# Kernel tuning notes

Hardware: AMD Instinct MI355X
Metric: run time of the kernel (lower is better)

## Reference

```python
import jax, jax.numpy as jnp
import numpy as np

IOU_THRESHOLD = 0.5
CLASS_CONF_THRESHOLD = 0.01
MAX_OUTPUT = 100  # tf.image.non_max_suppression max_output_size


def _nms_indices(boxes, scores, max_out, iou_thr):
    """Fixed-size greedy NMS: returns (idxs[max_out], valid[max_out])."""
    x1, y1, x2, y2 = boxes[:, 0], boxes[:, 1], boxes[:, 2], boxes[:, 3]
    areas = (x2 - x1) * (y2 - y1)

    def body(sc, _):
        i = jnp.argmax(sc)
        valid = sc[i] > 0.0  # score_threshold = 0.0 in tf call
        xx1 = jnp.maximum(x1[i], x1)
        yy1 = jnp.maximum(y1[i], y1)
        xx2 = jnp.minimum(x2[i], x2)
        yy2 = jnp.minimum(y2[i], y2)
        inter = jnp.maximum(xx2 - xx1, 0.0) * jnp.maximum(yy2 - yy1, 0.0)
        union = areas[i] + areas - inter
        iou = jnp.where(union > 0.0, inter / union, 0.0)
        # suppress overlapping boxes (self included, iou=1) only if pick valid
        sc_new = jnp.where((iou > iou_thr) & valid, -1.0, sc)
        return sc_new, (i, valid)

    _, (idxs, valids) = jax.lax.scan(body, scores, None, length=max_out)
    return idxs, valids


def _decode(x, anchors):
    B, H, W, A, C = x.shape  # B == 1
    gw = jnp.float32(W)
    # grid offsets: (col, row) per cell, matching cell_x / transposed cell_y
    cx = jnp.broadcast_to(jnp.arange(W, dtype=jnp.float32).reshape(1, 1, W, 1, 1), (1, H, W, 1, 1))
    cy = jnp.broadcast_to(jnp.arange(H, dtype=jnp.float32).reshape(1, H, 1, 1, 1), (1, H, W, 1, 1))
    grid = jnp.concatenate([cx, cy], axis=-1)  # (1,H,W,1,2)

    xy = (jax.nn.sigmoid(x[..., 0:2]) + grid) / gw                      # (B,H,W,A,2)
    wh = jnp.exp(x[..., 2:4]) * anchors.reshape(1, 1, 1, A, 2) / gw     # (B,H,W,A,2)
    boxes = jnp.concatenate([xy - wh / 2.0, xy + wh / 2.0], axis=-1)    # (B,H,W,A,4)

    conf = jax.nn.sigmoid(x[..., 4:5])                                  # (B,H,W,A,1)
    cls_prob = jax.nn.softmax(x[..., 5:], axis=-1)                      # (B,H,W,A,C-5)
    class_confidence = conf * cls_prob
    masked = jnp.where(class_confidence > CLASS_CONF_THRESHOLD, class_confidence, 0.0)
    classes = jnp.argmax(masked, axis=-1).astype(jnp.int32)             # (B,H,W,A)
    confm = jnp.max(masked, axis=-1)                                    # (B,H,W,A)

    N = H * W * A
    return boxes.reshape(N, 4), confm.reshape(N), classes.reshape(N)


def reference(x, anchors):
    boxes, scores, classes = _decode(x, anchors)
    idxs, valids = _nms_indices(jax.lax.stop_gradient(boxes),
                                jax.lax.stop_gradient(scores),
                                MAX_OUTPUT, IOU_THRESHOLD)
    sel_conf = jnp.where(valids, scores[idxs], 0.0)
    sel_boxes = jnp.where(valids[:, None], boxes[idxs], 0.0)
    sel_classes = jnp.where(valids, classes[idxs], -1)
    return sel_conf, sel_boxes, sel_classes


def setup_inputs() -> dict:
    key = jax.random.key(0)
    k1, k2 = jax.random.split(key)
    x = jax.random.normal(k1, (1, 256, 256, 5, 85), dtype=jnp.float32)
    # anchor priors in grid units (positive widths/heights)
    anchors = jax.random.uniform(k2, (5, 2), dtype=jnp.float32) * 4.0 + 0.5
    return {"x": x, "anchors": anchors}
```

## Files before the change

kernel.cpp:

```cpp
#include <hip/hip_runtime.h>
#include <hip/hip_bf16.h>

#define NROW 327680
#define NCLS 80
#define K_TARGET 1024u
#define CAP 2048u
#define MAXN 2048
#define MAX_OUT 100
#define NBIN 864
#define BIN0 0x3C23
#define HIST_BLOCKS 80
#define ADJW 32
#define ADJC_ROWS 128

#define WS_SCORES 0
#define WS_PART   1310720
#define WS_CNT    1587200
#define WS_KEYS   1587264
#define WS_SORT   1603648
#define WS_CBOX   1620032
#define WS_ADJ    1652800

typedef float f4v __attribute__((ext_vector_type(4)));
typedef f4v f4u __attribute__((aligned(4)));
typedef unsigned long long ull;

__global__ __launch_bounds__(256, 1) void decode_score(
    const float* __restrict__ x, float* __restrict__ scores) {
  const int r = blockIdx.x * 256 + threadIdx.x;
  const float* rp = x + (size_t)r * 85;

  float conf_l = rp[4];
  float cl[80];
  #pragma unroll
  for (int c = 0; c < 20; ++c) {
    f4v t4 = *(const f4u*)(rp + 5 + 4 * c);
    cl[4*c+0] = t4.x; cl[4*c+1] = t4.y; cl[4*c+2] = t4.z; cl[4*c+3] = t4.w;
  }

  float m = cl[0];
  #pragma unroll
  for (int c = 1; c < NCLS; ++c) { float l = cl[c]; if (l > m) m = l; }
  float s = 0.f;
  #pragma unroll
  for (int c = 0; c < NCLS; ++c) s += expf(cl[c] - m);
  float conf = 1.f / (1.f + expf(-conf_l));
  float best = conf * (1.f / s);
  scores[r] = (best > 0.01f) ? best : 0.f;
}

__global__ __launch_bounds__(1024) void hist_kernel(
    const float* __restrict__ scores, unsigned* __restrict__ part) {
  __shared__ unsigned h[NBIN];
  const int t = threadIdx.x;
  if (t < NBIN) h[t] = 0;
  __syncthreads();

  float4 s4 = ((const float4*)scores)[blockIdx.x * 1024 + t];
  float sv[4] = {s4.x, s4.y, s4.z, s4.w};
  #pragma unroll
  for (int k = 0; k < 4; ++k) {
    float s = sv[k];
    if (s > 0.f) {
      int idx = (int)(__float_as_uint(s) >> 16) - BIN0;
      if (idx > NBIN - 1) idx = NBIN - 1;
      atomicAdd(&h[idx], 1u);
    }
  }
  __syncthreads();
  if (t < NBIN) part[blockIdx.x * NBIN + t] = h[t];
}

__global__ __launch_bounds__(1024) void thresh_kernel(
    const unsigned* __restrict__ part, unsigned* __restrict__ cnt) {
  __shared__ unsigned bufA[1024], bufB[1024];
  const int t = threadIdx.x;

  unsigned colsum = 0;
  if (t < NBIN) {
    unsigned a0 = 0, a1 = 0, a2 = 0, a3 = 0;
    #pragma unroll
    for (int b = 0; b < HIST_BLOCKS; b += 4) {
      a0 += part[(b + 0) * NBIN + t];
      a1 += part[(b + 1) * NBIN + t];
      a2 += part[(b + 2) * NBIN + t];
      a3 += part[(b + 3) * NBIN + t];
    }
    colsum = a0 + a1 + a2 + a3;
  }
  bufA[t] = colsum;
  __syncthreads();

  unsigned* src = bufA; unsigned* dst = bufB;
  for (int d = 1; d < 1024; d <<= 1) {
    unsigned val = src[t] + ((t + d < 1024) ? src[t + d] : 0u);
    dst[t] = val;
    __syncthreads();
    unsigned* tmp = src; src = dst; dst = tmp;
  }
  if (src[t] >= K_TARGET && (t == 1023 || src[t + 1] < K_TARGET)) {
    unsigned T = (unsigned)t;
    if (src[t] > CAP) T += 1;
    cnt[1] = T;
  }
  if (t == 0) {
    if (src[0] < K_TARGET) cnt[1] = 0;
    cnt[0] = 0;
  }
}

__global__ __launch_bounds__(256) void compact_kernel(
    const float* __restrict__ scores, unsigned* __restrict__ cnt,
    ull* __restrict__ keys) {
  __shared__ unsigned blocal, bbase;
  const int t = threadIdx.x;
  if (t == 0) blocal = 0;
  __syncthreads();

  const unsigned T = cnt[1];
  const int gi = blockIdx.x * 256 + t;
  float4 s4 = ((const float4*)scores)[gi];
  float sv[4] = {s4.x, s4.y, s4.z, s4.w};
  ull lk[4]; int nl = 0;
  #pragma unroll
  for (int k = 0; k < 4; ++k) {
    float s = sv[k];
    if (s <= 0.f) continue;
    unsigned bits = __float_as_uint(s);
    int idx = (int)(bits >> 16) - BIN0;
    if (idx > NBIN - 1) idx = NBIN - 1;
    if ((unsigned)idx < T) continue;
    unsigned r = (unsigned)(gi * 4 + k);
    lk[nl++] = ((ull)bits << 32) | (ull)(0xFFFFFFFFu - r);
  }
  unsigned lpos = nl ? atomicAdd(&blocal, (unsigned)nl) : 0u;
  __syncthreads();
  if (t == 0 && blocal) bbase = atomicAdd(&cnt[0], blocal);
  __syncthreads();
  if (nl) {
    unsigned base = bbase + lpos;
    for (int i = 0; i < nl; ++i)
      if (base + i < CAP) keys[base + i] = lk[i];
  }
}

__global__ __launch_bounds__(64) void rank_kernel(
    const float* __restrict__ x, const float* __restrict__ anchors,
    const unsigned* __restrict__ cnt, const ull* __restrict__ keys,
    ull* __restrict__ sorted, float4* __restrict__ cboxg) {
  __shared__ ull lk[MAXN];
  unsigned n = cnt[0]; if (n > CAP) n = CAP;
  const int t = threadIdx.x;
  for (unsigned i = t; i < n; i += 64) lk[i] = keys[i];
  __syncthreads();

  const unsigned i = blockIdx.x * 64 + t;
  if (i >= n) return;
  const ull ki = lk[i];
  unsigned rank = 0;
  #pragma unroll 4
  for (unsigned j = 0; j < n; ++j) rank += (lk[j] > ki) ? 1u : 0u;

  sorted[rank] = ki;

  unsigned r = 0xFFFFFFFFu - (unsigned)(ki & 0xFFFFFFFFull);
  const float* rp = x + (size_t)r * 85;
  float tx = rp[0], ty = rp[1], tw = rp[2], th = rp[3];
  const int a  = (int)(r % 5u);
  const int hw = (int)(r / 5u);
  const float wf = (float)(hw & 255);
  const float hf = (float)(hw >> 8);
  float sx = 1.f / (1.f + expf(-tx));
  float sy = 1.f / (1.f + expf(-ty));
  float xc = (sx + wf) / 256.f;
  float yc = (sy + hf) / 256.f;
  float bw = expf(tw) * anchors[2*a]     / 256.f;
  float bh = expf(th) * anchors[2*a + 1] / 256.f;
  float hwd = bw / 2.f, hhd = bh / 2.f;
  cboxg[rank] = make_float4(xc - hwd, yc - hhd, xc + hwd, yc + hhd);
}

__global__ __launch_bounds__(256) void adj_kernel(
    const unsigned* __restrict__ cnt, const float4* __restrict__ cboxg,
    ull* __restrict__ adj) {
  unsigned n = cnt[0]; if (n > CAP) n = CAP;
  const unsigned i = blockIdx.x;
  if (i >= n) return;
  const float4 bi = cboxg[i];
  const float areai = (bi.z - bi.x) * (bi.w - bi.y);
  const int t = threadIdx.x, wid = t >> 6, lane = t & 63;

  #pragma unroll
  for (int pass = 0; pass < 8; ++pass) {
    unsigned j = (unsigned)(pass * 256 + t);
    bool sup = false;
    if (j < n) {
      float4 bj = cboxg[j];
      float xx1 = fmaxf(bi.x, bj.x), yy1 = fmaxf(bi.y, bj.y);
      float xx2 = fminf(bi.z, bj.z), yy2 = fminf(bi.w, bj.w);
      float inter = fmaxf(xx2 - xx1, 0.f) * fmaxf(yy2 - yy1, 0.f);
      float areaj = (bj.z - bj.x) * (bj.w - bj.y);
      float uni = areai + areaj - inter;
      float iou = (uni > 0.f) ? (inter / uni) : 0.f;
      sup = iou > 0.5f;
    }
    ull m = __ballot(sup);
    if (lane == 0) adj[(size_t)i * ADJW + pass * 4 + wid] = m;
  }
}

__global__ __launch_bounds__(1024) void final_kernel(
    const float* __restrict__ x, const unsigned* __restrict__ cnt,
    const ull* __restrict__ sorted, const float4* __restrict__ cboxg,
    const ull* __restrict__ adjg, float* __restrict__ out) {
  __shared__ ull sk[MAXN];
  __shared__ ull adjc[ADJC_ROWS * ADJW];
  __shared__ int keptcc[MAX_OUT];
  __shared__ int kcls[MAX_OUT];
  __shared__ int knum;
  const int t = threadIdx.x;
  if (t == 0) knum = 0;

  unsigned n = cnt[0]; if (n > CAP) n = CAP;
  for (unsigned i = t; i < n; i += 1024) sk[i] = sorted[i];
  const unsigned ncache = (n < ADJC_ROWS ? n : ADJC_ROWS) * ADJW;
  for (unsigned i = t; i < ncache; i += 1024) adjc[i] = adjg[i];
  __syncthreads();

  if (t < 64) {
    const int lane = t;
    ull mask = 0ull;
    int nk = 0;
    ull rA = 0ull, rB = 0ull;
    if (lane < ADJW) {
      if (n > 0) rA = adjc[0 * ADJW + lane];
      if (n > 1) rB = (1 < ADJC_ROWS) ? adjc[1 * ADJW + lane]
                                      : adjg[1 * ADJW + lane];
    }
    for (unsigned cc = 0; cc < n; ++cc) {
      ull rC = 0ull;
      unsigned pcc = cc + 2;
      if (lane < ADJW && pcc < n)
        rC = (pcc < ADJC_ROWS) ? adjc[pcc * ADJW + lane]
                               : adjg[(size_t)pcc * ADJW + lane];
      const int w = (int)(cc >> 6);
      ull mw = (ull)__shfl((long long)mask, w, 64);
      bool sup = (mw >> (cc & 63u)) & 1ull;
      if (!sup) {
        mask |= rA;
        if (lane == 0) keptcc[nk] = (int)cc;
        ++nk;
        if (nk == MAX_OUT) break;
      }
      rA = rB; rB = rC;
    }
    if (lane == 0) knum = nk;
  }
  __syncthreads();
  const int kn = knum;

  {
    const int wv = t >> 6, lane = t & 63;
    for (int kidx = wv; kidx < kn; kidx += 16) {
      ull key = sk[keptcc[kidx]];
      unsigned r = 0xFFFFFFFFu - (unsigned)(key & 0xFFFFFFFFull);
      const float* rp = x + (size_t)r * 85;
      float l0 = rp[5 + lane];
      unsigned b0 = __float_as_uint(l0);
      b0 = (b0 & 0x80000000u) ? ~b0 : (b0 | 0x80000000u);
      ull kv = ((ull)b0 << 32) | (ull)(0xFFFFFFFFu - lane);
      if (lane < 16) {
        float l1 = rp[5 + 64 + lane];
        unsigned b1 = __float_as_uint(l1);
        b1 = (b1 & 0x80000000u) ? ~b1 : (b1 | 0x80000000u);
        ull kv1 = ((ull)b1 << 32) | (ull)(0xFFFFFFFFu - (64 + lane));
        if (kv1 > kv) kv = kv1;
      }
      #pragma unroll
      for (int d = 32; d >= 1; d >>= 1) {
        ull o = (ull)__shfl_xor((long long)kv, d, 64);
        if (o > kv) kv = o;
      }
      if (lane == 0)
        kcls[kidx] = (int)(0xFFFFFFFFu - (unsigned)(kv & 0xFFFFFFFFull));
    }
  }
  __syncthreads();

  if (t < MAX_OUT) {
    float conf = 0.f; float4 bb = make_float4(0.f, 0.f, 0.f, 0.f); float cf = -1.f;
    if (t < kn) {
      int cc = keptcc[t];
      ull key = sk[cc];
      conf = __uint_as_float((unsigned)(key >> 32));
      bb = cboxg[cc];
      cf = (float)kcls[t];
    }
    out[t] = conf;
    ((float4*)(out + 100))[t] = bb;
    out[500 + t] = cf;
  }
}

extern "C" void kernel_launch(void* const* d_in, const int* in_sizes, int n_in,
                              void* d_out, int out_size, void* d_ws, size_t ws_size,
                              hipStream_t stream) {
  const float* x       = (const float*)d_in[0];
  const float* anchors = (const float*)d_in[1];
  float* out = (float*)d_out;
  char* ws = (char*)d_ws;

  float*    scores = (float*)(ws + WS_SCORES);
  unsigned* part   = (unsigned*)(ws + WS_PART);
  unsigned* cnt    = (unsigned*)(ws + WS_CNT);
  ull*      keys   = (ull*)(ws + WS_KEYS);
  ull*      sorted = (ull*)(ws + WS_SORT);
  float4*   cboxg  = (float4*)(ws + WS_CBOX);
  ull*      adj    = (ull*)(ws + WS_ADJ);

  hipLaunchKernelGGL(decode_score, dim3(NROW / 256), dim3(256),
                     0, stream, x, scores);
  hipLaunchKernelGGL(hist_kernel, dim3(HIST_BLOCKS), dim3(1024),
                     0, stream, scores, part);
  hipLaunchKernelGGL(thresh_kernel, dim3(1), dim3(1024), 0, stream, part, cnt);
  hipLaunchKernelGGL(compact_kernel, dim3(NROW / 1024), dim3(256),
                     0, stream, scores, cnt, keys);
  hipLaunchKernelGGL(rank_kernel, dim3(MAXN / 64), dim3(64),
                     0, stream, x, anchors, cnt, keys, sorted, cboxg);
  hipLaunchKernelGGL(adj_kernel, dim3(MAXN), dim3(256),
                     0, stream, cnt, cboxg, adj);
  hipLaunchKernelGGL(final_kernel, dim3(1), dim3(1024), 0, stream,
                     x, cnt, sorted, cboxg, adj, out);
}
```

Before: 236.1 us.

## Fuse histogram into decode and merge later stages into one cooperative kernel

Each decode block now builds a shared-memory histogram of its scores and writes a per-block partial, which removes the separate histogram pass over the score array. Threshold, compaction, ranking, box decode, IoU adjacency and greedy NMS now run in one cooperative kernel of 80 blocks, separated by grid syncs, instead of five launches. Ranking and adjacency are spread one wavefront per row across all blocks. This cuts launch overhead, at the cost of grid-sync latency and a fixed grid of 80 blocks that must all be co-resident.

```diff
diff --git a/kernel.cpp b/kernel.cpp
--- a/kernel.cpp
+++ b/kernel.cpp
@@ -1,5 +1,5 @@
 #include <hip/hip_runtime.h>
-#include <hip/hip_bf16.h>
+#include <hip/hip_cooperative_groups.h>
 
 #define NROW 327680
 #define NCLS 80
@@ -9,25 +9,32 @@
 #define MAX_OUT 100
 #define NBIN 864
 #define BIN0 0x3C23
-#define HIST_BLOCKS 80
+#define DEC_BLOCKS 1280
 #define ADJW 32
 #define ADJC_ROWS 128
 
 #define WS_SCORES 0
 #define WS_PART   1310720
-#define WS_CNT    1587200
-#define WS_KEYS   1587264
-#define WS_SORT   1603648
-#define WS_CBOX   1620032
-#define WS_ADJ    1652800
+#define WS_HIST   5734400
+#define WS_CNT    5738496
+#define WS_KEYS   5738560
+#define WS_SORT   5754944
+#define WS_CBOX   5771328
+#define WS_ADJ    5804096
 
 typedef float f4v __attribute__((ext_vector_type(4)));
 typedef f4v f4u __attribute__((aligned(4)));
 typedef unsigned long long ull;
 
-__global__ __launch_bounds__(256, 1) void decode_score(
-    const float* __restrict__ x, float* __restrict__ scores) {
-  const int r = blockIdx.x * 256 + threadIdx.x;
+__global__ __launch_bounds__(256, 1) void decode_hist(
+    const float* __restrict__ x, float* __restrict__ scores,
+    unsigned* __restrict__ part) {
+  __shared__ unsigned h[NBIN];
+  const int t = threadIdx.x;
+  for (int i = t; i < NBIN; i += 256) h[i] = 0;
+  __syncthreads();
+
+  const int r = blockIdx.x * 256 + t;
   const float* rp = x + (size_t)r * 85;
 
   float conf_l = rp[4];
@@ -37,7 +44,6 @@
     f4v t4 = *(const f4u*)(rp + 5 + 4 * c);
     cl[4*c+0] = t4.x; cl[4*c+1] = t4.y; cl[4*c+2] = t4.z; cl[4*c+3] = t4.w;
   }
-
   float m = cl[0];
   #pragma unroll
   for (int c = 1; c < NCLS; ++c) { float l = cl[c]; if (l > m) m = l; }
@@ -46,51 +52,53 @@
   for (int c = 0; c < NCLS; ++c) s += expf(cl[c] - m);
   float conf = 1.f / (1.f + expf(-conf_l));
   float best = conf * (1.f / s);
-  scores[r] = (best > 0.01f) ? best : 0.f;
+  float score = (best > 0.01f) ? best : 0.f;
+  scores[r] = score;
+
+  if (score > 0.f) {
+    int idx = (int)(__float_as_uint(score) >> 16) - BIN0;
+    if (idx > NBIN - 1) idx = NBIN - 1;
+    atomicAdd(&h[idx], 1u);
+  }
+  __syncthreads();
+  unsigned* pb = part + (size_t)blockIdx.x * NBIN;
+  for (int i = t; i < NBIN; i += 256) pb[i] = h[i];
 }
 
-__global__ __launch_bounds__(1024) void hist_kernel(
-    const float* __restrict__ scores, unsigned* __restrict__ part) {
-  __shared__ unsigned h[NBIN];
+__global__ __launch_bounds__(1024) void coop_kernel(
+    const float* __restrict__ x, const float* __restrict__ anchors,
+    const float* __restrict__ scores, const unsigned* __restrict__ part,
+    unsigned* __restrict__ hist, unsigned* __restrict__ cnt,
+    ull* __restrict__ keys, ull* __restrict__ sorted,
+    float4* __restrict__ cboxs, ull* __restrict__ adj,
+    float* __restrict__ out) {
+  cooperative_groups::grid_group gg = cooperative_groups::this_grid();
   const int t = threadIdx.x;
-  if (t < NBIN) h[t] = 0;
-  __syncthreads();
-
-  float4 s4 = ((const float4*)scores)[blockIdx.x * 1024 + t];
-  float sv[4] = {s4.x, s4.y, s4.z, s4.w};
-  #pragma unroll
-  for (int k = 0; k < 4; ++k) {
-    float s = sv[k];
-    if (s > 0.f) {
-      int idx = (int)(__float_as_uint(s) >> 16) - BIN0;
-      if (idx > NBIN - 1) idx = NBIN - 1;
-      atomicAdd(&h[idx], 1u);
-    }
-  }
-  __syncthreads();
-  if (t < NBIN) part[blockIdx.x * NBIN + t] = h[t];
-}
-
-__global__ __launch_bounds__(1024) void thresh_kernel(
-    const unsigned* __restrict__ part, unsigned* __restrict__ cnt) {
+  const int b = blockIdx.x;
+  const int wv = t >> 6, lane = t & 63;
+
   __shared__ unsigned bufA[1024], bufB[1024];
-  const int t = threadIdx.x;
-
-  unsigned colsum = 0;
+  __shared__ unsigned TshL, blocal, bbase;
+  __shared__ ull lk[MAXN];
+  __shared__ ull adjc[ADJC_ROWS * ADJW];
+  __shared__ int keptcc[MAX_OUT];
+  __shared__ int kcls[MAX_OUT];
+  __shared__ int knum;
+
+  if (b == 0) { if (t < NBIN) hist[t] = 0u; if (t < 2) cnt[t] = 0u; }
+  gg.sync();
+
   if (t < NBIN) {
-    unsigned a0 = 0, a1 = 0, a2 = 0, a3 = 0;
+    unsigned s = 0;
     #pragma unroll
-    for (int b = 0; b < HIST_BLOCKS; b += 4) {
-      a0 += part[(b + 0) * NBIN + t];
-      a1 += part[(b + 1) * NBIN + t];
-      a2 += part[(b + 2) * NBIN + t];
-      a3 += part[(b + 3) * NBIN + t];
-    }
-    colsum = a0 + a1 + a2 + a3;
-  }
-  bufA[t] = colsum;
-  __syncthreads();
-
+    for (int k = 0; k < 16; ++k)
+      s += part[(size_t)(b * 16 + k) * NBIN + t];
+    if (s) atomicAdd(&hist[t], s);
+  }
+  gg.sync();
+
+  bufA[t] = (t < NBIN) ? hist[t] : 0u;
+  __syncthreads();
   unsigned* src = bufA; unsigned* dst = bufB;
   for (int d = 1; d < 1024; d <<= 1) {
     unsigned val = src[t] + ((t + d < 1024) ? src[t + d] : 0u);
@@ -99,150 +107,120 @@
     unsigned* tmp = src; src = dst; dst = tmp;
   }
   if (src[t] >= K_TARGET && (t == 1023 || src[t + 1] < K_TARGET)) {
-    unsigned T = (unsigned)t;
-    if (src[t] > CAP) T += 1;
-    cnt[1] = T;
-  }
-  if (t == 0) {
-    if (src[0] < K_TARGET) cnt[1] = 0;
-    cnt[0] = 0;
-  }
-}
-
-__global__ __launch_bounds__(256) void compact_kernel(
-    const float* __restrict__ scores, unsigned* __restrict__ cnt,
-    ull* __restrict__ keys) {
-  __shared__ unsigned blocal, bbase;
-  const int t = threadIdx.x;
+    unsigned TT = (unsigned)t;
+    if (src[t] > CAP) TT += 1;
+    TshL = TT;
+  }
+  if (t == 0 && src[0] < K_TARGET) TshL = 0;
+  __syncthreads();
+  const unsigned T = TshL;
+
   if (t == 0) blocal = 0;
   __syncthreads();
-
-  const unsigned T = cnt[1];
-  const int gi = blockIdx.x * 256 + t;
-  float4 s4 = ((const float4*)scores)[gi];
-  float sv[4] = {s4.x, s4.y, s4.z, s4.w};
-  ull lk[4]; int nl = 0;
-  #pragma unroll
-  for (int k = 0; k < 4; ++k) {
-    float s = sv[k];
-    if (s <= 0.f) continue;
-    unsigned bits = __float_as_uint(s);
-    int idx = (int)(bits >> 16) - BIN0;
-    if (idx > NBIN - 1) idx = NBIN - 1;
-    if ((unsigned)idx < T) continue;
-    unsigned r = (unsigned)(gi * 4 + k);
-    lk[nl++] = ((ull)bits << 32) | (ull)(0xFFFFFFFFu - r);
-  }
-  unsigned lpos = nl ? atomicAdd(&blocal, (unsigned)nl) : 0u;
-  __syncthreads();
-  if (t == 0 && blocal) bbase = atomicAdd(&cnt[0], blocal);
-  __syncthreads();
-  if (nl) {
-    unsigned base = bbase + lpos;
-    for (int i = 0; i < nl; ++i)
-      if (base + i < CAP) keys[base + i] = lk[i];
-  }
-}
-
-__global__ __launch_bounds__(64) void rank_kernel(
-    const float* __restrict__ x, const float* __restrict__ anchors,
-    const unsigned* __restrict__ cnt, const ull* __restrict__ keys,
-    ull* __restrict__ sorted, float4* __restrict__ cboxg) {
-  __shared__ ull lk[MAXN];
+  {
+    const int gi = b * 1024 + t;
+    float4 s4 = ((const float4*)scores)[gi];
+    float sv[4] = {s4.x, s4.y, s4.z, s4.w};
+    ull lkk[4]; int nl = 0;
+    #pragma unroll
+    for (int k = 0; k < 4; ++k) {
+      float s = sv[k];
+      if (s <= 0.f) continue;
+      unsigned bits = __float_as_uint(s);
+      int idx = (int)(bits >> 16) - BIN0;
+      if (idx > NBIN - 1) idx = NBIN - 1;
+      if ((unsigned)idx < T) continue;
+      unsigned r = (unsigned)(gi * 4 + k);
+      lkk[nl++] = ((ull)bits << 32) | (ull)(0xFFFFFFFFu - r);
+    }
+    unsigned lpos = nl ? atomicAdd(&blocal, (unsigned)nl) : 0u;
+    __syncthreads();
+    if (t == 0 && blocal) bbase = atomicAdd(&cnt[0], blocal);
+    __syncthreads();
+    if (nl) {
+      unsigned base = bbase + lpos;
+      for (int i2 = 0; i2 < nl; ++i2)
+        if (base + i2 < CAP) keys[base + i2] = lkk[i2];
+    }
+  }
+  gg.sync();
+
   unsigned n = cnt[0]; if (n > CAP) n = CAP;
-  const int t = threadIdx.x;
-  for (unsigned i = t; i < n; i += 64) lk[i] = keys[i];
-  __syncthreads();
-
-  const unsigned i = blockIdx.x * 64 + t;
-  if (i >= n) return;
-  const ull ki = lk[i];
-  unsigned rank = 0;
-  #pragma unroll 4
-  for (unsigned j = 0; j < n; ++j) rank += (lk[j] > ki) ? 1u : 0u;
-
-  sorted[rank] = ki;
-
-  unsigned r = 0xFFFFFFFFu - (unsigned)(ki & 0xFFFFFFFFull);
-  const float* rp = x + (size_t)r * 85;
-  float tx = rp[0], ty = rp[1], tw = rp[2], th = rp[3];
-  const int a  = (int)(r % 5u);
-  const int hw = (int)(r / 5u);
-  const float wf = (float)(hw & 255);
-  const float hf = (float)(hw >> 8);
-  float sx = 1.f / (1.f + expf(-tx));
-  float sy = 1.f / (1.f + expf(-ty));
-  float xc = (sx + wf) / 256.f;
-  float yc = (sy + hf) / 256.f;
-  float bw = expf(tw) * anchors[2*a]     / 256.f;
-  float bh = expf(th) * anchors[2*a + 1] / 256.f;
-  float hwd = bw / 2.f, hhd = bh / 2.f;
-  cboxg[rank] = make_float4(xc - hwd, yc - hhd, xc + hwd, yc + hhd);
-}
-
-__global__ __launch_bounds__(256) void adj_kernel(
-    const unsigned* __restrict__ cnt, const float4* __restrict__ cboxg,
-    ull* __restrict__ adj) {
-  unsigned n = cnt[0]; if (n > CAP) n = CAP;
-  const unsigned i = blockIdx.x;
-  if (i >= n) return;
-  const float4 bi = cboxg[i];
-  const float areai = (bi.z - bi.x) * (bi.w - bi.y);
-  const int t = threadIdx.x, wid = t >> 6, lane = t & 63;
-
-  #pragma unroll
-  for (int pass = 0; pass < 8; ++pass) {
-    unsigned j = (unsigned)(pass * 256 + t);
-    bool sup = false;
-    if (j < n) {
-      float4 bj = cboxg[j];
-      float xx1 = fmaxf(bi.x, bj.x), yy1 = fmaxf(bi.y, bj.y);
-      float xx2 = fminf(bi.z, bj.z), yy2 = fminf(bi.w, bj.w);
-      float inter = fmaxf(xx2 - xx1, 0.f) * fmaxf(yy2 - yy1, 0.f);
-      float areaj = (bj.z - bj.x) * (bj.w - bj.y);
-      float uni = areai + areaj - inter;
-      float iou = (uni > 0.f) ? (inter / uni) : 0.f;
-      sup = iou > 0.5f;
-    }
-    ull m = __ballot(sup);
-    if (lane == 0) adj[(size_t)i * ADJW + pass * 4 + wid] = m;
-  }
-}
-
-__global__ __launch_bounds__(1024) void final_kernel(
-    const float* __restrict__ x, const unsigned* __restrict__ cnt,
-    const ull* __restrict__ sorted, const float4* __restrict__ cboxg,
-    const ull* __restrict__ adjg, float* __restrict__ out) {
-  __shared__ ull sk[MAXN];
-  __shared__ ull adjc[ADJC_ROWS * ADJW];
-  __shared__ int keptcc[MAX_OUT];
-  __shared__ int kcls[MAX_OUT];
-  __shared__ int knum;
-  const int t = threadIdx.x;
+
+  for (unsigned i = t; i < n; i += 1024) lk[i] = keys[i];
+  __syncthreads();
+  for (unsigned i = b * 16u + wv; i < n; i += 1280u) {
+    ull ki = lk[i];
+    unsigned rk = 0;
+    for (unsigned j = lane; j < n; j += 64) rk += (lk[j] > ki) ? 1u : 0u;
+    #pragma unroll
+    for (int d2 = 32; d2 >= 1; d2 >>= 1) rk += __shfl_xor((int)rk, d2, 64);
+    if (lane == 0) {
+      sorted[rk] = ki;
+      unsigned r = 0xFFFFFFFFu - (unsigned)(ki & 0xFFFFFFFFull);
+      const float* rp = x + (size_t)r * 85;
+      float tx = rp[0], ty = rp[1], tw = rp[2], th = rp[3];
+      const int a  = (int)(r % 5u);
+      const int hw = (int)(r / 5u);
+      const float wf = (float)(hw & 255);
+      const float hf = (float)(hw >> 8);
+      float sx = 1.f / (1.f + expf(-tx));
+      float sy = 1.f / (1.f + expf(-ty));
+      float xc = (sx + wf) / 256.f;
+      float yc = (sy + hf) / 256.f;
+      float bw = expf(tw) * anchors[2*a]     / 256.f;
+      float bh = expf(th) * anchors[2*a + 1] / 256.f;
+      float hwd = bw / 2.f, hhd = bh / 2.f;
+      cboxs[rk] = make_float4(xc - hwd, yc - hhd, xc + hwd, yc + hhd);
+    }
+  }
+  gg.sync();
+
+  for (unsigned i = b * 16u + wv; i < n; i += 1280u) {
+    float4 bi = cboxs[i];
+    float areai = (bi.z - bi.x) * (bi.w - bi.y);
+    for (unsigned it = 0; it < ADJW; ++it) {
+      unsigned j = it * 64u + lane;
+      bool sup = false;
+      if (j < n) {
+        float4 bj = cboxs[j];
+        float xx1 = fmaxf(bi.x, bj.x), yy1 = fmaxf(bi.y, bj.y);
+        float xx2 = fminf(bi.z, bj.z), yy2 = fminf(bi.w, bj.w);
+        float inter = fmaxf(xx2 - xx1, 0.f) * fmaxf(yy2 - yy1, 0.f);
+        float areaj = (bj.z - bj.x) * (bj.w - bj.y);
+        float uni = areai + areaj - inter;
+        float iou = (uni > 0.f) ? (inter / uni) : 0.f;
+        sup = iou > 0.5f;
+      }
+      ull mm = __ballot(sup);
+      if (lane == 0) adj[(size_t)i * ADJW + it] = mm;
+    }
+  }
+  gg.sync();
+
+  if (b != 0) return;
+
   if (t == 0) knum = 0;
-
-  unsigned n = cnt[0]; if (n > CAP) n = CAP;
-  for (unsigned i = t; i < n; i += 1024) sk[i] = sorted[i];
+  for (unsigned i = t; i < n; i += 1024) lk[i] = sorted[i];
   const unsigned ncache = (n < ADJC_ROWS ? n : ADJC_ROWS) * ADJW;
-  for (unsigned i = t; i < ncache; i += 1024) adjc[i] = adjg[i];
+  for (unsigned i = t; i < ncache; i += 1024) adjc[i] = adj[i];
   __syncthreads();
 
   if (t < 64) {
-    const int lane = t;
     ull mask = 0ull;
     int nk = 0;
     ull rA = 0ull, rB = 0ull;
     if (lane < ADJW) {
       if (n > 0) rA = adjc[0 * ADJW + lane];
       if (n > 1) rB = (1 < ADJC_ROWS) ? adjc[1 * ADJW + lane]
-                                      : adjg[1 * ADJW + lane];
+                                      : adj[1 * ADJW + lane];
     }
     for (unsigned cc = 0; cc < n; ++cc) {
       ull rC = 0ull;
       unsigned pcc = cc + 2;
       if (lane < ADJW && pcc < n)
         rC = (pcc < ADJC_ROWS) ? adjc[pcc * ADJW + lane]
-                               : adjg[(size_t)pcc * ADJW + lane];
+                               : adj[(size_t)pcc * ADJW + lane];
       const int w = (int)(cc >> 6);
       ull mw = (ull)__shfl((long long)mask, w, 64);
       bool sup = (mw >> (cc & 63u)) & 1ull;
@@ -259,31 +237,28 @@
   __syncthreads();
   const int kn = knum;
 
-  {
-    const int wv = t >> 6, lane = t & 63;
-    for (int kidx = wv; kidx < kn; kidx += 16) {
-      ull key = sk[keptcc[kidx]];
-      unsigned r = 0xFFFFFFFFu - (unsigned)(key & 0xFFFFFFFFull);
-      const float* rp = x + (size_t)r * 85;
-      float l0 = rp[5 + lane];
-      unsigned b0 = __float_as_uint(l0);
-      b0 = (b0 & 0x80000000u) ? ~b0 : (b0 | 0x80000000u);
-      ull kv = ((ull)b0 << 32) | (ull)(0xFFFFFFFFu - lane);
-      if (lane < 16) {
-        float l1 = rp[5 + 64 + lane];
-        unsigned b1 = __float_as_uint(l1);
-        b1 = (b1 & 0x80000000u) ? ~b1 : (b1 | 0x80000000u);
-        ull kv1 = ((ull)b1 << 32) | (ull)(0xFFFFFFFFu - (64 + lane));
-        if (kv1 > kv) kv = kv1;
-      }
-      #pragma unroll
-      for (int d = 32; d >= 1; d >>= 1) {
-        ull o = (ull)__shfl_xor((long long)kv, d, 64);
-        if (o > kv) kv = o;
-      }
-      if (lane == 0)
-        kcls[kidx] = (int)(0xFFFFFFFFu - (unsigned)(kv & 0xFFFFFFFFull));
-    }
+  for (int kidx = wv; kidx < kn; kidx += 16) {
+    ull key = lk[keptcc[kidx]];
+    unsigned r = 0xFFFFFFFFu - (unsigned)(key & 0xFFFFFFFFull);
+    const float* rp = x + (size_t)r * 85;
+    float l0 = rp[5 + lane];
+    unsigned b0 = __float_as_uint(l0);
+    b0 = (b0 & 0x80000000u) ? ~b0 : (b0 | 0x80000000u);
+    ull kv = ((ull)b0 << 32) | (ull)(0xFFFFFFFFu - lane);
+    if (lane < 16) {
+      float l1 = rp[5 + 64 + lane];
+      unsigned b1 = __float_as_uint(l1);
+      b1 = (b1 & 0x80000000u) ? ~b1 : (b1 | 0x80000000u);
+      ull kv1 = ((ull)b1 << 32) | (ull)(0xFFFFFFFFu - (64 + lane));
+      if (kv1 > kv) kv = kv1;
+    }
+    #pragma unroll
+    for (int d3 = 32; d3 >= 1; d3 >>= 1) {
+      ull o = (ull)__shfl_xor((long long)kv, d3, 64);
+      if (o > kv) kv = o;
+    }
+    if (lane == 0)
+      kcls[kidx] = (int)(0xFFFFFFFFu - (unsigned)(kv & 0xFFFFFFFFull));
   }
   __syncthreads();
 
@@ -291,9 +266,9 @@
     float conf = 0.f; float4 bb = make_float4(0.f, 0.f, 0.f, 0.f); float cf = -1.f;
     if (t < kn) {
       int cc = keptcc[t];
-      ull key = sk[cc];
+      ull key = lk[cc];
       conf = __uint_as_float((unsigned)(key >> 32));
-      bb = cboxg[cc];
+      bb = cboxs[cc];
       cf = (float)kcls[t];
     }
     out[t] = conf;
@@ -312,23 +287,19 @@
 
   float*    scores = (float*)(ws + WS_SCORES);
   unsigned* part   = (unsigned*)(ws + WS_PART);
+  unsigned* hist   = (unsigned*)(ws + WS_HIST);
   unsigned* cnt    = (unsigned*)(ws + WS_CNT);
   ull*      keys   = (ull*)(ws + WS_KEYS);
   ull*      sorted = (ull*)(ws + WS_SORT);
-  float4*   cboxg  = (float4*)(ws + WS_CBOX);
+  float4*   cboxs  = (float4*)(ws + WS_CBOX);
   ull*      adj    = (ull*)(ws + WS_ADJ);
 
-  hipLaunchKernelGGL(decode_score, dim3(NROW / 256), dim3(256),
-                     0, stream, x, scores);
-  hipLaunchKernelGGL(hist_kernel, dim3(HIST_BLOCKS), dim3(1024),
-                     0, stream, scores, part);
-  hipLaunchKernelGGL(thresh_kernel, dim3(1), dim3(1024), 0, stream, part, cnt);
-  hipLaunchKernelGGL(compact_kernel, dim3(NROW / 1024), dim3(256),
-                     0, stream, scores, cnt, keys);
-  hipLaunchKernelGGL(rank_kernel, dim3(MAXN / 64), dim3(64),
-                     0, stream, x, anchors, cnt, keys, sorted, cboxg);
-  hipLaunchKernelGGL(adj_kernel, dim3(MAXN), dim3(256),
-                     0, stream, cnt, cboxg, adj);
-  hipLaunchKernelGGL(final_kernel, dim3(1), dim3(1024), 0, stream,
-                     x, cnt, sorted, cboxg, adj, out);
+  hipLaunchKernelGGL(decode_hist, dim3(DEC_BLOCKS), dim3(256),
+                     0, stream, x, scores, part);
+
+  void* kargs[] = { (void*)&x, (void*)&anchors, (void*)&scores, (void*)&part,
+                    (void*)&hist, (void*)&cnt, (void*)&keys, (void*)&sorted,
+                    (void*)&cboxs, (void*)&adj, (void*)&out };
+  hipLaunchCooperativeKernel((void*)coop_kernel, dim3(80), dim3(1024),
+                             kargs, 0, stream);
 }
```

After: 272.2 us. +15.3%, slower.
